# Kernel tuning notes

Hardware: AMD Instinct MI355X
Metric: run time of the kernel (lower is better)

## Reference

```python
import jax, jax.numpy as jnp
import numpy as np
import math

VOCAB = 50000
EMB_DIM = 300
D_MODEL = 2048
BATCH = 4
SEQ = 8192


def setup_inputs() -> dict:
    key = jax.random.key(0)
    k1, k2, k3, k4 = jax.random.split(key, 4)
    x = jax.random.randint(k1, (BATCH, SEQ), 0, VOCAB, dtype=jnp.int64 if jax.config.jax_enable_x64 else jnp.int32)
    emb = jax.random.normal(k2, (VOCAB, EMB_DIM), dtype=jnp.float32)
    # nn.Linear(300, d_model): weight [d_model, 300] in torch; store transposed [300, d_model]
    W = jax.random.normal(k3, (EMB_DIM, D_MODEL), dtype=jnp.float32) * (1.0 / math.sqrt(EMB_DIM))
    b = jax.random.normal(k4, (D_MODEL,), dtype=jnp.float32) * 0.01
    return {"x": x, "emb": emb, "W": W, "b": b}


def reference(x, emb, W, b):
    # Dict lookup per token == single gather: [B, S] -> [B, S, 300]
    vecs = emb[x]
    # Linear(300 -> d_model) then scale by sqrt(d_model)
    out = jnp.einsum("bse,ed->bsd", vecs, W) + b
    return out * jnp.sqrt(jnp.asarray(W.shape[1], dtype=out.dtype))
```

## Files before the change

### kernel.cpp

```cpp
#include <hip/hip_runtime.h>
#include <hip/hip_bf16.h>


#define TOKENS 32768
#define EMB 300
#define DM 2048
#define KPAD 320
#define SCALE 45.25483399593904f

typedef _Float16 f16;
typedef _Float16 h4 __attribute__((ext_vector_type(4)));
typedef _Float16 h8 __attribute__((ext_vector_type(8)));
typedef float f32x4 __attribute__((ext_vector_type(4)));

__global__ __launch_bounds__(256) void prep_w(const float* __restrict__ W, f16* __restrict__ Wt) {
    __shared__ f16 tile[64 * 68];
    const int k0 = blockIdx.x << 6;
    const int n0 = blockIdx.y << 6;
    const int t = threadIdx.x;
    #pragma unroll
    for (int i = 0; i < 4; ++i) {
        int idx = (i << 8) + t;
        int kr = idx >> 4;
        int nc = idx & 15;
        h4 hv = {};
        if (k0 + kr < EMB) {
            float4 v = *(const float4*)(W + (size_t)(k0 + kr) * DM + n0 + (nc << 2));
            hv[0]=(f16)v.x; hv[1]=(f16)v.y; hv[2]=(f16)v.z; hv[3]=(f16)v.w;
        }
        *(h4*)(tile + kr * 68 + (nc << 2)) = hv;
    }
    __syncthreads();
    #pragma unroll
    for (int i = 0; i < 4; ++i) {
        int idx = (i << 8) + t;
        int n  = idx >> 4;
        int kc = idx & 15;
        h4 hv;
        hv[0] = tile[(kc * 4 + 0) * 68 + n];
        hv[1] = tile[(kc * 4 + 1) * 68 + n];
        hv[2] = tile[(kc * 4 + 2) * 68 + n];
        hv[3] = tile[(kc * 4 + 3) * 68 + n];
        *(h4*)(Wt + (size_t)(n0 + n) * KPAD + k0 + (kc << 2)) = hv;
    }
}

__global__ __launch_bounds__(256) void prep_b(const float* __restrict__ b, float* __restrict__ bs) {
    int i = blockIdx.x * 256 + threadIdx.x;
    if (i < DM) bs[i] = b[i] * SCALE;
}

__global__ __launch_bounds__(256, 4) void embed_gemm(
        const int* __restrict__ x, const float* __restrict__ emb,
        const f16* __restrict__ Wt, const float* __restrict__ bs,
        float* __restrict__ out)
{
    __shared__ __align__(16) f16 As[128 * 64];
    __shared__ __align__(16) f16 Bs[128 * 64];
    __shared__ int toks[128];

    const int lin  = blockIdx.x;
    const int xcd  = lin & 7;
    const int slot = lin >> 3;
    const int mtile = (xcd << 5) + (slot >> 4);
    const int ntile = slot & 15;
    const int m0 = mtile << 7;
    const int n0 = ntile << 7;

    const int t = threadIdx.x;
    const int lane = t & 63;
    const int wave = t >> 6;
    const int wm = (wave >> 1) << 6;
    const int wn = (wave & 1) << 6;
    const int quad = lane >> 4;
    const int lr = lane & 15;

    if (t < 128) toks[t] = x[m0 + t];
    __syncthreads();

    f32x4 acc[4][4] = {};

    for (int kc = 0; kc < 5; ++kc) {
        const int k0 = kc << 6;

        #pragma unroll
        for (int i = 0; i < 4; ++i) {
            int idx = (i << 8) + t;
            int row = idx >> 3;
            int c   = idx & 7;
            h8 v = *(const h8*)(Wt + (size_t)(n0 + row) * KPAD + k0 + (c << 3));
            *(h8*)(Bs + (row << 6) + ((c ^ (row & 7)) << 3)) = v;
        }

        #pragma unroll
        for (int i = 0; i < 8; ++i) {
            int q   = (i << 8) + t;
            int row = q >> 4;
            int qc  = q & 15;
            int k   = k0 + (qc << 2);
            h4 hv = {};
            if (k + 3 < EMB) {
                float4 v = *(const float4*)(emb + (size_t)toks[row] * EMB + k);
                hv[0]=(f16)v.x; hv[1]=(f16)v.y; hv[2]=(f16)v.z; hv[3]=(f16)v.w;
            }
            int c = qc >> 1, half = qc & 1;
            *(h4*)(As + (row << 6) + (((c ^ (row & 7)) << 3) + (half << 2))) = hv;
        }
        __syncthreads();

        #pragma unroll
        for (int kk = 0; kk < 2; ++kk) {
            h8 af[4], bfr[4];
            const int c = (kk << 2) + quad;
            #pragma unroll
            for (int mi = 0; mi < 4; ++mi) {
                int m = wm + (mi << 4) + lr;
                af[mi] = *(const h8*)(As + (m << 6) + ((c ^ (m & 7)) << 3));
            }
            #pragma unroll
            for (int ni = 0; ni < 4; ++ni) {
                int n = wn + (ni << 4) + lr;
                bfr[ni] = *(const h8*)(Bs + (n << 6) + ((c ^ (n & 7)) << 3));
            }
            #pragma unroll
            for (int mi = 0; mi < 4; ++mi)
                #pragma unroll
                for (int ni = 0; ni < 4; ++ni)
                    acc[mi][ni] = __builtin_amdgcn_mfma_f32_16x16x32_f16(
                        af[mi], bfr[ni], acc[mi][ni], 0, 0, 0);
        }
        __syncthreads();
    }

    #pragma unroll
    for (int ni = 0; ni < 4; ++ni) {
        int n = n0 + wn + (ni << 4) + lr;
        float bias = bs[n];
        #pragma unroll
        for (int mi = 0; mi < 4; ++mi) {
            int mb = m0 + wm + (mi << 4) + (quad << 2);
            #pragma unroll
            for (int r = 0; r < 4; ++r) {
                out[(size_t)(mb + r) * DM + n] = fmaf(acc[mi][ni][r], SCALE, bias);
            }
        }
    }
}

__global__ __launch_bounds__(256) void naive_kernel(
        const int* __restrict__ x, const float* __restrict__ emb,
        const float* __restrict__ W, const float* __restrict__ b, float* __restrict__ out)
{
    size_t idx = (size_t)blockIdx.x * 256 + threadIdx.x;
    int n = (int)(idx & (DM - 1));
    size_t m = idx >> 11;
    const float* e = emb + (size_t)x[m] * EMB;
    float a = 0.f;
    for (int k = 0; k < EMB; ++k) a = fmaf(e[k], W[(size_t)k * DM + n], a);
    out[idx] = (a + b[n]) * SCALE;
}

extern "C" void kernel_launch(void* const* d_in, const int* in_sizes, int n_in,
                              void* d_out, int out_size, void* d_ws, size_t ws_size,
                              hipStream_t stream) {
    const int*   x   = (const int*)d_in[0];
    const float* emb = (const float*)d_in[1];
    const float* W   = (const float*)d_in[2];
    const float* b   = (const float*)d_in[3];
    float* out = (float*)d_out;

    const size_t wt_bytes = (size_t)DM * KPAD * sizeof(f16);
    const size_t need = wt_bytes + (size_t)DM * sizeof(float);

    if (ws_size >= need) {
        f16* Wt = (f16*)d_ws;
        float* bsp = (float*)((char*)d_ws + wt_bytes);
        prep_w<<<dim3(KPAD / 64, DM / 64), 256, 0, stream>>>(W, Wt);
        prep_b<<<DM / 256, 256, 0, stream>>>(b, bsp);
        embed_gemm<<<(TOKENS / 128) * (DM / 128), 256, 0, stream>>>(x, emb, Wt, bsp, out);
    } else {
        naive_kernel<<<((size_t)TOKENS * DM) / 256, 256, 0, stream>>>(x, emb, W, b, out);
    }
}
```

Measured before the change: 416.4 us.

## Pre-convert embedding table to fp16 and stream tiles via global_load_lds

Adds a prep pass that converts the whole 50000x300 fp32 embedding table into a padded fp16 table, and a prep pass that lays W out in pre-swizzled tile order. The GEMM then loads both A and B tiles directly into LDS with global_load_lds 16-byte transfers, dropping the per-tile fp32 gather and convert and the register round trip. This removes repeated conversion work, since each gathered row was converted 16 times across n-tiles. In exchange it converts the full vocab (about 60MB read and 32MB written) every call, even though only the used rows matter, and it needs a larger workspace.

```diff
diff --git a/kernel.cpp b/kernel.cpp
--- a/kernel.cpp
+++ b/kernel.cpp
@@ -1,7 +1,7 @@
 #include <hip/hip_runtime.h>
-#include <hip/hip_bf16.h>
-
-
+
+
+#define VOCAB 50000
 #define TOKENS 32768
 #define EMB 300
 #define DM 2048
@@ -13,7 +13,149 @@
 typedef _Float16 h8 __attribute__((ext_vector_type(8)));
 typedef float f32x4 __attribute__((ext_vector_type(4)));
 
-__global__ __launch_bounds__(256) void prep_w(const float* __restrict__ W, f16* __restrict__ Wt) {
+__device__ __forceinline__ void gload_lds16(const f16* g, f16* l) {
+    __builtin_amdgcn_global_load_lds(
+        (const __attribute__((address_space(1))) void*)g,
+        (__attribute__((address_space(3))) void*)l, 16, 0, 0);
+}
+
+__global__ __launch_bounds__(256) void prep_emb(const float* __restrict__ emb,
+                                                f16* __restrict__ embh) {
+    int idx = blockIdx.x * 256 + threadIdx.x;
+    if (idx >= VOCAB * 40) return;
+    int row = idx / 40;
+    int c = idx - row * 40;
+    h8 hv = {};
+    const float* src = emb + (size_t)row * EMB + (c << 3);
+    if (c < 37) {
+        float4 a = *(const float4*)src;
+        float4 d = *(const float4*)(src + 4);
+        hv[0]=(f16)a.x; hv[1]=(f16)a.y; hv[2]=(f16)a.z; hv[3]=(f16)a.w;
+        hv[4]=(f16)d.x; hv[5]=(f16)d.y; hv[6]=(f16)d.z; hv[7]=(f16)d.w;
+    } else if (c == 37) {
+        float4 a = *(const float4*)src;
+        hv[0]=(f16)a.x; hv[1]=(f16)a.y; hv[2]=(f16)a.z; hv[3]=(f16)a.w;
+    }
+    *(h8*)(embh + (size_t)row * KPAD + (c << 3)) = hv;
+}
+
+__global__ __launch_bounds__(256) void prep_wsw(const float* __restrict__ W,
+                                                f16* __restrict__ Wsw) {
+    int idx = blockIdx.x * 256 + threadIdx.x;
+    int p = idx & 1023;
+    int tile = idx >> 10;
+    int kc = tile % 5;
+    int ntile = tile / 5;
+    int row = p >> 3, cpos = p & 7;
+    int clog = cpos ^ (row & 7);
+    int n = (ntile << 7) + row;
+    int kbase = (kc << 6) + (clog << 3);
+    h8 hv = {};
+    #pragma unroll
+    for (int j = 0; j < 8; ++j) {
+        int k = kbase + j;
+        if (k < EMB) hv[j] = (f16)W[(size_t)k * DM + n];
+    }
+    *(h8*)(Wsw + (size_t)idx * 8) = hv;
+}
+
+__global__ __launch_bounds__(256) void prep_b(const float* __restrict__ b, float* __restrict__ bs) {
+    int i = blockIdx.x * 256 + threadIdx.x;
+    if (i < DM) bs[i] = b[i] * SCALE;
+}
+
+__global__ __launch_bounds__(256, 4) void embed_gemm(
+        const int* __restrict__ x, const f16* __restrict__ embh,
+        const f16* __restrict__ Wsw, const float* __restrict__ bs,
+        float* __restrict__ out)
+{
+    __shared__ __align__(16) f16 As[128 * 64];
+    __shared__ __align__(16) f16 Bs[128 * 64];
+    __shared__ int toks[128];
+
+    const int lin  = blockIdx.x;
+    const int xcd  = lin & 7;
+    const int slot = lin >> 3;
+    const int mtile = (xcd << 5) + (slot >> 4);
+    const int ntile = slot & 15;
+    const int m0 = mtile << 7;
+    const int n0 = ntile << 7;
+
+    const int t = threadIdx.x;
+    const int lane = t & 63;
+    const int wave = t >> 6;
+    const int wm = (wave >> 1) << 6;
+    const int wn = (wave & 1) << 6;
+    const int quad = lane >> 4;
+    const int lr = lane & 15;
+
+    if (t < 128) toks[t] = x[m0 + t];
+    __syncthreads();
+
+    const int arow_lo = t >> 3;
+    const int axor = ((t & 7) ^ (arow_lo & 7)) << 3;
+    const f16* asrc[4];
+    #pragma unroll
+    for (int i = 0; i < 4; ++i)
+        asrc[i] = embh + (size_t)toks[(i << 5) + arow_lo] * KPAD + axor;
+
+    const f16* bsrc = Wsw + (size_t)ntile * 40960 + ((size_t)t << 3);
+
+    f16* adst = As + (t << 3);
+    f16* bdst = Bs + (t << 3);
+
+    f32x4 acc[4][4] = {};
+
+    for (int kc = 0; kc < 5; ++kc) {
+        const int koff = kc << 6;
+        #pragma unroll
+        for (int i = 0; i < 4; ++i)
+            gload_lds16(bsrc + (kc << 13) + (i << 11), bdst + (i << 11));
+        #pragma unroll
+        for (int i = 0; i < 4; ++i)
+            gload_lds16(asrc[i] + koff, adst + (i << 11));
+        __syncthreads();
+
+        #pragma unroll
+        for (int kk = 0; kk < 2; ++kk) {
+            h8 af[4], bfr[4];
+            const int c = (kk << 2) + quad;
+            #pragma unroll
+            for (int mi = 0; mi < 4; ++mi) {
+                int m = wm + (mi << 4) + lr;
+                af[mi] = *(const h8*)(As + (m << 6) + ((c ^ (m & 7)) << 3));
+            }
+            #pragma unroll
+            for (int ni = 0; ni < 4; ++ni) {
+                int n = wn + (ni << 4) + lr;
+                bfr[ni] = *(const h8*)(Bs + (n << 6) + ((c ^ (n & 7)) << 3));
+            }
+            #pragma unroll
+            for (int mi = 0; mi < 4; ++mi)
+                #pragma unroll
+                for (int ni = 0; ni < 4; ++ni)
+                    acc[mi][ni] = __builtin_amdgcn_mfma_f32_16x16x32_f16(
+                        af[mi], bfr[ni], acc[mi][ni], 0, 0, 0);
+        }
+        __syncthreads();
+    }
+
+    #pragma unroll
+    for (int ni = 0; ni < 4; ++ni) {
+        int n = n0 + wn + (ni << 4) + lr;
+        float bias = bs[n];
+        #pragma unroll
+        for (int mi = 0; mi < 4; ++mi) {
+            int mb = m0 + wm + (mi << 4) + (quad << 2);
+            #pragma unroll
+            for (int r = 0; r < 4; ++r) {
+                out[(size_t)(mb + r) * DM + n] = fmaf(acc[mi][ni][r], SCALE, bias);
+            }
+        }
+    }
+}
+
+__global__ __launch_bounds__(256) void prep_w_old(const float* __restrict__ W, f16* __restrict__ Wt) {
     __shared__ f16 tile[64 * 68];
     const int k0 = blockIdx.x << 6;
     const int n0 = blockIdx.y << 6;
@@ -45,12 +187,7 @@
     }
 }
 
-__global__ __launch_bounds__(256) void prep_b(const float* __restrict__ b, float* __restrict__ bs) {
-    int i = blockIdx.x * 256 + threadIdx.x;
-    if (i < DM) bs[i] = b[i] * SCALE;
-}
-
-__global__ __launch_bounds__(256, 4) void embed_gemm(
+__global__ __launch_bounds__(256, 4) void embed_gemm_old(
         const int* __restrict__ x, const float* __restrict__ emb,
         const f16* __restrict__ Wt, const float* __restrict__ bs,
         float* __restrict__ out)
@@ -82,7 +219,6 @@
 
     for (int kc = 0; kc < 5; ++kc) {
         const int k0 = kc << 6;
-
         #pragma unroll
         for (int i = 0; i < 4; ++i) {
             int idx = (i << 8) + t;
@@ -91,7 +227,6 @@
             h8 v = *(const h8*)(Wt + (size_t)(n0 + row) * KPAD + k0 + (c << 3));
             *(h8*)(Bs + (row << 6) + ((c ^ (row & 7)) << 3)) = v;
         }
-
         #pragma unroll
         for (int i = 0; i < 8; ++i) {
             int q   = (i << 8) + t;
@@ -169,15 +304,25 @@
     const float* b   = (const float*)d_in[3];
     float* out = (float*)d_out;
 
-    const size_t wt_bytes = (size_t)DM * KPAD * sizeof(f16);
-    const size_t need = wt_bytes + (size_t)DM * sizeof(float);
-
-    if (ws_size >= need) {
+    const size_t embh_bytes = (size_t)VOCAB * KPAD * sizeof(f16);
+    const size_t wsw_bytes  = (size_t)DM * KPAD * sizeof(f16);
+    const size_t need_big   = embh_bytes + wsw_bytes + (size_t)DM * sizeof(float);
+    const size_t need_small = wsw_bytes + (size_t)DM * sizeof(float);
+
+    if (ws_size >= need_big) {
+        f16* embh = (f16*)d_ws;
+        f16* Wsw  = (f16*)((char*)d_ws + embh_bytes);
+        float* bsp = (float*)((char*)d_ws + embh_bytes + wsw_bytes);
+        prep_emb<<<(VOCAB * 40 + 255) / 256, 256, 0, stream>>>(emb, embh);
+        prep_wsw<<<(16 * 5 * 1024) / 256, 256, 0, stream>>>(W, Wsw);
+        prep_b<<<DM / 256, 256, 0, stream>>>(b, bsp);
+        embed_gemm<<<(TOKENS / 128) * (DM / 128), 256, 0, stream>>>(x, embh, Wsw, bsp, out);
+    } else if (ws_size >= need_small) {
         f16* Wt = (f16*)d_ws;
-        float* bsp = (float*)((char*)d_ws + wt_bytes);
-        prep_w<<<dim3(KPAD / 64, DM / 64), 256, 0, stream>>>(W, Wt);
+        float* bsp = (float*)((char*)d_ws + wsw_bytes);
+        prep_w_old<<<dim3(KPAD / 64, DM / 64), 256, 0, stream>>>(W, Wt);
         prep_b<<<DM / 256, 256, 0, stream>>>(b, bsp);
-        embed_gemm<<<(TOKENS / 128) * (DM / 128), 256, 0, stream>>>(x, emb, Wt, bsp, out);
+        embed_gemm_old<<<(TOKENS / 128) * (DM / 128), 256, 0, stream>>>(x, emb, Wt, bsp, out);
     } else {
         naive_kernel<<<((size_t)TOKENS * DM) / 256, 256, 0, stream>>>(x, emb, W, b, out);
     }
```

Measured after the change: 393.7 us. 5.5% less time.
